# Performance work log

Hardware: AMD Instinct MI355X
Metric: run time of the kernel (lower is better)

## Reference

```python
import jax, jax.numpy as jnp
import numpy as np

B, N, DH = 8, 2048, 512
EPS = 1e-5


def _layer_norm(x, g, b):
    m = x.mean(-1, keepdims=True)
    v = ((x - m) ** 2).mean(-1, keepdims=True)
    return (x - m) * jax.lax.rsqrt(v + EPS) * g + b


def setup_inputs() -> dict:
    key = jax.random.key(0)
    ks = jax.random.split(key, 20)
    s = 1.0 / np.sqrt(DH)
    sf = 1.0 / np.sqrt(2 * DH)
    return {
        "H": jax.random.normal(ks[0], (B, N, DH), jnp.float32),
        "adj": jax.random.uniform(ks[1], (B, N, N), jnp.float32),
        "hop_emb": jax.random.normal(ks[2], (N, DH), jnp.float32),
        "Wq": jax.random.normal(ks[3], (DH, DH), jnp.float32) * s,
        "bq": jnp.zeros((DH,), jnp.float32),
        "Wk": jax.random.normal(ks[4], (DH, DH), jnp.float32) * s,
        "bk": jnp.zeros((DH,), jnp.float32),
        "Wv": jax.random.normal(ks[5], (DH, DH), jnp.float32) * s,
        "bv": jnp.zeros((DH,), jnp.float32),
        "W1": jax.random.normal(ks[6], (DH, 2 * DH), jnp.float32) * s,
        "b1": jnp.zeros((2 * DH,), jnp.float32),
        "W2": jax.random.normal(ks[7], (2 * DH, DH), jnp.float32) * sf,
        "b2": jnp.zeros((DH,), jnp.float32),
        "g1": jnp.ones((DH,), jnp.float32),
        "be1": jnp.zeros((DH,), jnp.float32),
        "g2": jnp.ones((DH,), jnp.float32),
        "be2": jnp.zeros((DH,), jnp.float32),
    }


def reference(H, adj, hop_emb, Wq, bq, Wk, bk, Wv, bv, W1, b1, W2, b2, g1, be1, g2, be2):
    Q = H @ Wq + bq                                     # [B,N,DH]
    K = H @ Wk + bk
    V = H @ Wv + bv
    scores = jnp.einsum("bid,bjd->bij", Q, K) / np.sqrt(DH).astype(np.float32)
    # (adj[...,None] * hop_emb).mean(-1) == adj * hop_emb.mean(-1)[j]
    hop_effect = adj * hop_emb.mean(-1)[None, None, :]  # [B,N,N]
    attn = jax.nn.softmax(scores * hop_effect, axis=-1)
    attn_out = jnp.einsum("bij,bjd->bid", attn, V)
    x = _layer_norm(attn_out + H, g1, be1)
    ffn = jax.nn.relu(x @ W1 + b1) @ W2 + b2
    return _layer_norm(ffn + x, g2, be2)
```

## Files before the change

### kernel.cpp

```cpp
#include <hip/hip_runtime.h>

typedef unsigned short u16;
typedef __bf16 bf16x8 __attribute__((ext_vector_type(8)));
typedef float f32x4 __attribute__((ext_vector_type(4)));

#define SEQN 2048
#define DHID 512

static __device__ __forceinline__ float bf2f(u16 u) {
    union { unsigned int i; float f; } c; c.i = ((unsigned int)u) << 16; return c.f;
}
static __device__ __forceinline__ u16 f2bf(float f) {
    union { float f; unsigned int i; } c; c.f = f;
    unsigned int x = c.i;
    return (u16)((x + 0x7fffu + ((x >> 16) & 1u)) >> 16);
}

static __device__ __forceinline__ void gld_lds16(const u16* g, u16* l) {
    __builtin_amdgcn_global_load_lds(
        (__attribute__((address_space(1))) void*)(g),
        (__attribute__((address_space(3))) void*)(l), 16, 0, 0);
}

__global__ __launch_bounds__(256) void cvt_kernel(const float* __restrict__ src,
                                                  u16* __restrict__ dst, int n) {
    int i = (blockIdx.x * 256 + threadIdx.x) * 8;
    if (i >= n) return;
    float4 a = *(const float4*)(src + i);
    float4 b = *(const float4*)(src + i + 4);
    union { uint4 u; u16 s[8]; } o;
    o.s[0] = f2bf(a.x); o.s[1] = f2bf(a.y); o.s[2] = f2bf(a.z); o.s[3] = f2bf(a.w);
    o.s[4] = f2bf(b.x); o.s[5] = f2bf(b.y); o.s[6] = f2bf(b.z); o.s[7] = f2bf(b.w);
    *(uint4*)(dst + i) = o.u;
}

__global__ __launch_bounds__(256) void cvt_t_kernel(const float* __restrict__ src,
                                                    u16* __restrict__ dst, int K, int N) {
    int idx = blockIdx.x * 256 + threadIdx.x;
    if (idx >= K * N) return;
    int n = idx / K, k = idx - n * K;
    dst[idx] = f2bf(src[(size_t)k * N + n]);
}

__global__ void hmean_kernel(const float* __restrict__ hop, float* __restrict__ hm) {
    int j = blockIdx.x, t = threadIdx.x;
    const float* p = hop + (size_t)j * DHID + t * 8;
    float4 a = *(const float4*)p;
    float4 b = *(const float4*)(p + 4);
    float s = a.x + a.y + a.z + a.w + b.x + b.y + b.z + b.w;
#pragma unroll
    for (int m = 1; m < 64; m <<= 1) s += __shfl_xor(s, m);
    if (t == 0) hm[j] = s * (1.0f / (float)DHID);
}

enum { EPI_BIAS = 0, EPI_RELU = 1, EPI_PLAIN = 3, EPI_BIAS_T = 4 };

template <int EPI>
__global__ __launch_bounds__(256) void gemm_bt(
    const u16* __restrict__ A, const u16* __restrict__ Bt, u16* __restrict__ C,
    const float* __restrict__ bias,
    int K, int lda, int ldb, int ldc,
    long sA, long sB, long sC)
{
    __shared__ u16 As[128 * 32];
    __shared__ u16 Bs[128 * 32];

    const int tid = threadIdx.x;
    const int bz = blockIdx.z;
    const u16* Ab = A + (size_t)bz * sA;
    const u16* Bb = Bt + (size_t)bz * sB;
    u16* Cb = C + (size_t)bz * sC;

    const int bm0 = blockIdx.y * 128, bn0 = blockIdx.x * 128;
    const int wid = tid >> 6, lane = tid & 63, quad = lane >> 4, l16 = lane & 15;
    const int wm = (wid >> 1) * 64, wn = (wid & 1) * 64;
    const int srow = lane >> 2;
    const int skof = (lane & 3) * 8;

    f32x4 acc[4][4];
#pragma unroll
    for (int i = 0; i < 4; ++i)
#pragma unroll
        for (int j = 0; j < 4; ++j) acc[i][j] = (f32x4){0.f, 0.f, 0.f, 0.f};

    for (int k0 = 0; k0 < K; k0 += 32) {
#pragma unroll
        for (int it = 0; it < 2; ++it) {
            int c = wid * 2 + it;
            gld_lds16(Ab + (size_t)(bm0 + c * 16 + srow) * lda + k0 + skof,
                      &As[c * 512]);
        }
#pragma unroll
        for (int it = 0; it < 2; ++it) {
            int c = wid * 2 + it;
            gld_lds16(Bb + (size_t)(bn0 + c * 16 + srow) * ldb + k0 + skof,
                      &Bs[c * 512]);
        }
        __syncthreads();

        bf16x8 af[4], bfr[4];
#pragma unroll
        for (int i = 0; i < 4; ++i)
            af[i] = *(const bf16x8*)&As[(wm + i * 16 + l16) * 32 + quad * 8];
#pragma unroll
        for (int j = 0; j < 4; ++j)
            bfr[j] = *(const bf16x8*)&Bs[(wn + j * 16 + l16) * 32 + quad * 8];
#pragma unroll
        for (int i = 0; i < 4; ++i)
#pragma unroll
            for (int j = 0; j < 4; ++j)
                acc[i][j] = __builtin_amdgcn_mfma_f32_16x16x32_bf16(af[i], bfr[j], acc[i][j], 0, 0, 0);
        __syncthreads();
    }

#pragma unroll
    for (int i = 0; i < 4; ++i) {
#pragma unroll
        for (int j = 0; j < 4; ++j) {
            const int gn = bn0 + wn + j * 16 + l16;
            const int gm0 = bm0 + wm + i * 16 + quad * 4;
            if constexpr (EPI == EPI_BIAS || EPI == EPI_RELU) {
                const float b = bias[gn];
#pragma unroll
                for (int r = 0; r < 4; ++r) {
                    float v = acc[i][j][r] + b;
                    if constexpr (EPI == EPI_RELU) v = fmaxf(v, 0.f);
                    Cb[(size_t)(gm0 + r) * ldc + gn] = f2bf(v);
                }
            } else if constexpr (EPI == EPI_BIAS_T) {
                const float b = bias[gn];
                const int bb = gm0 >> 11, n = gm0 & 2047;
                ushort4 o;
                o.x = f2bf(acc[i][j][0] + b);
                o.y = f2bf(acc[i][j][1] + b);
                o.z = f2bf(acc[i][j][2] + b);
                o.w = f2bf(acc[i][j][3] + b);
                *(ushort4*)&C[((size_t)bb * 512 + gn) * 2048 + n] = o;
            } else {
#pragma unroll
                for (int r = 0; r < 4; ++r)
                    Cb[(size_t)(gm0 + r) * ldc + gn] = f2bf(acc[i][j][r]);
            }
        }
    }
}

__global__ __launch_bounds__(256, 1) void attn_kernel(
    const u16* __restrict__ Q, const u16* __restrict__ K, const u16* __restrict__ Vt,
    const float* __restrict__ adj, const float* __restrict__ hm,
    u16* __restrict__ AO)
{
    extern __shared__ u16 lds[];
    u16* Ks = lds;
    u16* Vs = lds + 16384;

    const int tid = threadIdx.x, wid = tid >> 6, lane = tid & 63;
    const int quad = lane >> 4, l16 = lane & 15;
    const int b = blockIdx.x;
    const int q0w = blockIdx.y * 64 + wid * 16;
    const int srow = lane >> 2, sko = (lane & 3) * 8;

    const u16* Qg = Q + (size_t)b * SEQN * DHID;
    const u16* Kg = K + (size_t)b * SEQN * DHID;
    const u16* Vg = Vt + (size_t)b * DHID * SEQN;
    const float* adjg = adj + (size_t)b * SEQN * SEQN;
    u16* AOg = AO + (size_t)b * SEQN * DHID;
    u16* Plds = lds + wid * 640;

    const float scale = 0.044194173824159216f;

    bf16x8 qf[16];
#pragma unroll
    for (int ds = 0; ds < 16; ++ds)
        qf[ds] = *(const bf16x8*)(Qg + (size_t)(q0w + l16) * DHID + ds * 32 + quad * 8);

    f32x4 oacc[32];
#pragma unroll
    for (int dt = 0; dt < 32; ++dt) oacc[dt] = (f32x4){0.f, 0.f, 0.f, 0.f};
    float lsum[4] = {0.f, 0.f, 0.f, 0.f};

    for (int kt = 0; kt < 64; ++kt) {
        const int kv0 = kt * 32;

#pragma unroll
        for (int i = 0; i < 8; ++i) {
            int id = wid * 8 + i;
            int ds = id >> 1, c = id & 1;
            gld_lds16(Kg + (size_t)(kv0 + c * 16 + srow) * DHID + ds * 32 + sko,
                      &Ks[ds * 1024 + c * 512]);
        }
        __syncthreads();

#pragma unroll
        for (int i = 0; i < 8; ++i) {
            int id = wid * 8 + i;
            gld_lds16(Vg + (size_t)(id * 16 + srow) * SEQN + kv0 + sko,
                      &Vs[id * 512]);
        }

        float hv0 = hm[kv0 + l16] * scale;
        float hv1 = hm[kv0 + 16 + l16] * scale;
        float av[8];
        const float* arow = adjg + (size_t)(q0w + quad * 4) * SEQN + kv0;
#pragma unroll
        for (int r = 0; r < 4; ++r) {
            av[r]     = arow[(size_t)r * SEQN + l16];
            av[4 + r] = arow[(size_t)r * SEQN + 16 + l16];
        }

        f32x4 s0a = {0.f,0.f,0.f,0.f}, s0b = {0.f,0.f,0.f,0.f};
        f32x4 s1a = {0.f,0.f,0.f,0.f}, s1b = {0.f,0.f,0.f,0.f};
#pragma unroll
        for (int ds = 0; ds < 16; ds += 2) {
            bf16x8 k00 = *(const bf16x8*)&Ks[ds * 1024 + l16 * 32 + quad * 8];
            bf16x8 k01 = *(const bf16x8*)&Ks[ds * 1024 + 512 + l16 * 32 + quad * 8];
            s0a = __builtin_amdgcn_mfma_f32_16x16x32_bf16(qf[ds], k00, s0a, 0, 0, 0);
            s1a = __builtin_amdgcn_mfma_f32_16x16x32_bf16(qf[ds], k01, s1a, 0, 0, 0);
            bf16x8 k10 = *(const bf16x8*)&Ks[(ds + 1) * 1024 + l16 * 32 + quad * 8];
            bf16x8 k11 = *(const bf16x8*)&Ks[(ds + 1) * 1024 + 512 + l16 * 32 + quad * 8];
            s0b = __builtin_amdgcn_mfma_f32_16x16x32_bf16(qf[ds + 1], k10, s0b, 0, 0, 0);
            s1b = __builtin_amdgcn_mfma_f32_16x16x32_bf16(qf[ds + 1], k11, s1b, 0, 0, 0);
        }
        f32x4 s0 = s0a + s0b, s1 = s1a + s1b;
        __syncthreads();

#pragma unroll
        for (int r = 0; r < 4; ++r) {
            float p0 = __expf(s0[r] * av[r] * hv0);
            float p1 = __expf(s1[r] * av[4 + r] * hv1);
            lsum[r] += p0 + p1;
            Plds[(quad * 4 + r) * 40 + l16] = f2bf(p0);
            Plds[(quad * 4 + r) * 40 + 16 + l16] = f2bf(p1);
        }
        asm volatile("s_waitcnt lgkmcnt(0)" ::: "memory");

        bf16x8 pf = *(const bf16x8*)&Plds[l16 * 40 + quad * 8];
#pragma unroll
        for (int dt = 0; dt < 32; ++dt) {
            bf16x8 vf = *(const bf16x8*)&Vs[(dt * 16 + l16) * 32 + quad * 8];
            oacc[dt] = __builtin_amdgcn_mfma_f32_16x16x32_bf16(pf, vf, oacc[dt], 0, 0, 0);
        }
        __syncthreads();
    }

#pragma unroll
    for (int r = 0; r < 4; ++r) {
#pragma unroll
        for (int m = 1; m < 16; m <<= 1) lsum[r] += __shfl_xor(lsum[r], m);
        lsum[r] = 1.f / lsum[r];
    }
#pragma unroll
    for (int dt = 0; dt < 32; ++dt) {
#pragma unroll
        for (int r = 0; r < 4; ++r) {
            AOg[(size_t)(q0w + quad * 4 + r) * DHID + dt * 16 + l16] =
                f2bf(oacc[dt][r] * lsum[r]);
        }
    }
}

template <bool B_F32, bool OUT_F32>
__global__ __launch_bounds__(256) void ln_kernel(
    const u16* __restrict__ a, const void* __restrict__ bp,
    const float* __restrict__ g, const float* __restrict__ be,
    void* __restrict__ out)
{
    size_t row = blockIdx.x;
    int t = threadIdx.x, wid = t >> 6, lane = t & 63;
    const u16* pa = a + row * (size_t)DHID;

    unsigned int va = *(const unsigned int*)(pa + t * 2);
    float b0, b1;
    if constexpr (B_F32) {
        float2 vb = *(const float2*)((const float*)bp + row * (size_t)DHID + t * 2);
        b0 = vb.x; b1 = vb.y;
    } else {
        unsigned int vb = *(const unsigned int*)((const u16*)bp + row * (size_t)DHID + t * 2);
        b0 = bf2f((u16)(vb & 0xffff)); b1 = bf2f((u16)(vb >> 16));
    }
    float x0 = bf2f((u16)(va & 0xffff)) + b0;
    float x1 = bf2f((u16)(va >> 16)) + b1;
    float s = x0 + x1, sq = x0 * x0 + x1 * x1;
#pragma unroll
    for (int m = 1; m < 64; m <<= 1) { s += __shfl_xor(s, m); sq += __shfl_xor(sq, m); }
    __shared__ float rs[4], rq[4];
    if (lane == 0) { rs[wid] = s; rq[wid] = sq; }
    __syncthreads();
    s = rs[0] + rs[1] + rs[2] + rs[3];
    sq = rq[0] + rq[1] + rq[2] + rq[3];
    float mean = s * (1.f / (float)DHID);
    float var = sq * (1.f / (float)DHID) - mean * mean;
    float rstd = rsqrtf(var + 1e-5f);

    float2 vg = *(const float2*)(g + t * 2);
    float2 vbe = *(const float2*)(be + t * 2);
    float y0 = (x0 - mean) * rstd * vg.x + vbe.x;
    float y1 = (x1 - mean) * rstd * vg.y + vbe.y;
    if constexpr (OUT_F32) {
        *(float2*)((float*)out + row * (size_t)DHID + t * 2) = make_float2(y0, y1);
    } else {
        unsigned int o = (unsigned int)f2bf(y0) | ((unsigned int)f2bf(y1) << 16);
        *(unsigned int*)((u16*)out + row * (size_t)DHID + t * 2) = o;
    }
}

extern "C" void kernel_launch(void* const* d_in, const int* in_sizes, int n_in,
                              void* d_out, int out_size, void* d_ws, size_t ws_size,
                              hipStream_t stream) {
    const float* H   = (const float*)d_in[0];
    const float* adj = (const float*)d_in[1];
    const float* hop = (const float*)d_in[2];
    const float* Wq  = (const float*)d_in[3];
    const float* bq  = (const float*)d_in[4];
    const float* Wk  = (const float*)d_in[5];
    const float* bk  = (const float*)d_in[6];
    const float* Wv  = (const float*)d_in[7];
    const float* bv  = (const float*)d_in[8];
    const float* W1  = (const float*)d_in[9];
    const float* b1  = (const float*)d_in[10];
    const float* W2  = (const float*)d_in[11];
    const float* b2  = (const float*)d_in[12];
    const float* g1  = (const float*)d_in[13];
    const float* be1 = (const float*)d_in[14];
    const float* g2  = (const float*)d_in[15];
    const float* be2 = (const float*)d_in[16];

    const size_t MiB = 1ull << 20;
    char* w = (char*)d_ws;
    float* hm  = (float*)w;
    u16* Hb   = (u16*)(w + 1 * MiB);
    u16* Wqt  = (u16*)(w + 17 * MiB);
    u16* Wkt  = (u16*)(w + 17 * MiB + 512 * 1024);
    u16* Wvt  = (u16*)(w + 18 * MiB);
    u16* W1t  = (u16*)(w + 18 * MiB + 512 * 1024);
    u16* W2t  = (u16*)(w + 19 * MiB + 512 * 1024);
    u16* Q    = (u16*)(w + 21 * MiB);
    u16* Kb   = (u16*)(w + 37 * MiB);
    u16* Vt   = (u16*)(w + 53 * MiB);
    u16* AO   = (u16*)(w + 69 * MiB);
    u16* HID  = (u16*)(w + 85 * MiB);
    u16* X   = Kb;
    u16* F2  = Vt;

    const int BN = 8, N = SEQN, D = DHID;
    const long nd = (long)N * D;

    cvt_kernel<<<(BN * N * D) / (8 * 256), 256, 0, stream>>>(H, Hb, BN * N * D);
    cvt_t_kernel<<<(D * D + 255) / 256, 256, 0, stream>>>(Wq, Wqt, D, D);
    cvt_t_kernel<<<(D * D + 255) / 256, 256, 0, stream>>>(Wk, Wkt, D, D);
    cvt_t_kernel<<<(D * D + 255) / 256, 256, 0, stream>>>(Wv, Wvt, D, D);
    cvt_t_kernel<<<(D * 2 * D + 255) / 256, 256, 0, stream>>>(W1, W1t, D, 2 * D);
    cvt_t_kernel<<<(2 * D * D + 255) / 256, 256, 0, stream>>>(W2, W2t, 2 * D, D);

    hmean_kernel<<<N, 64, 0, stream>>>(hop, hm);

    gemm_bt<EPI_BIAS><<<dim3(4, 128, 1), 256, 0, stream>>>(
        Hb, Wqt, Q, bq, D, D, D, D, 0, 0, 0);
    gemm_bt<EPI_BIAS><<<dim3(4, 128, 1), 256, 0, stream>>>(
        Hb, Wkt, Kb, bk, D, D, D, D, 0, 0, 0);
    gemm_bt<EPI_BIAS_T><<<dim3(4, 128, 1), 256, 0, stream>>>(
        Hb, Wvt, Vt, bv, D, D, D, D, 0, 0, 0);

    attn_kernel<<<dim3(8, 32), 256, 65536, stream>>>(Q, Kb, Vt, adj, hm, AO);

    ln_kernel<true, false><<<BN * N, 256, 0, stream>>>(AO, H, g1, be1, X);

    gemm_bt<EPI_RELU><<<dim3(8, 128, 1), 256, 0, stream>>>(
        X, W1t, HID, b1, D, D, D, 2 * D, 0, 0, 0);

    gemm_bt<EPI_BIAS><<<dim3(4, 128, 1), 256, 0, stream>>>(
        HID, W2t, F2, b2, 2 * D, 2 * D, 2 * D, D, 0, 0, 0);

    ln_kernel<false, true><<<BN * N, 256, 0, stream>>>(F2, X, g2, be2, (float*)d_out);
}
```

Measured before the change: 595.9 us.

## Fuse QKV projections into one GEMM and split attention over two KV halves

The three Q/K/V projection GEMMs become a single GEMM over a concatenated transposed weight, with an epilogue that routes each column tile to Q, K or transposed V. The attention kernel gets a second grid dimension that splits the key/value range in half. Each half writes unnormalized partial outputs and row sums, and the first LayerNorm kernel adds the halves and normalizes them. This is meant to double the number of attention blocks for better CU utilization and to cut launch and A-reload overhead for the projections. In exchange it adds extra partial-output traffic to global memory, and more blocks may not help if register or LDS use limits occupancy to one block per CU.

Measured after the change: 595.5 us. Within noise of the previous version (-0.1%).

```diff
diff --git a/kernel.cpp b/kernel.cpp
--- a/kernel.cpp
+++ b/kernel.cpp
@@ -53,23 +53,23 @@
     if (t == 0) hm[j] = s * (1.0f / (float)DHID);
 }
 
-enum { EPI_BIAS = 0, EPI_RELU = 1, EPI_PLAIN = 3, EPI_BIAS_T = 4 };
+enum { EPI_BIAS = 0, EPI_RELU = 1, EPI_PLAIN = 3, EPI_BIAS_T = 4, EPI_QKV = 5 };
 
 template <int EPI>
 __global__ __launch_bounds__(256) void gemm_bt(
     const u16* __restrict__ A, const u16* __restrict__ Bt, u16* __restrict__ C,
     const float* __restrict__ bias,
     int K, int lda, int ldb, int ldc,
-    long sA, long sB, long sC)
+    u16* __restrict__ Qo, u16* __restrict__ Ko, u16* __restrict__ Vto,
+    const float* __restrict__ bq_, const float* __restrict__ bk_,
+    const float* __restrict__ bv_)
 {
     __shared__ u16 As[128 * 32];
     __shared__ u16 Bs[128 * 32];
 
     const int tid = threadIdx.x;
-    const int bz = blockIdx.z;
-    const u16* Ab = A + (size_t)bz * sA;
-    const u16* Bb = Bt + (size_t)bz * sB;
-    u16* Cb = C + (size_t)bz * sC;
+    const u16* Ab = A;
+    const u16* Bb = Bt;
 
     const int bm0 = blockIdx.y * 128, bn0 = blockIdx.x * 128;
     const int wid = tid >> 6, lane = tid & 63, quad = lane >> 4, l16 = lane & 15;
@@ -125,7 +125,7 @@
                 for (int r = 0; r < 4; ++r) {
                     float v = acc[i][j][r] + b;
                     if constexpr (EPI == EPI_RELU) v = fmaxf(v, 0.f);
-                    Cb[(size_t)(gm0 + r) * ldc + gn] = f2bf(v);
+                    C[(size_t)(gm0 + r) * ldc + gn] = f2bf(v);
                 }
             } else if constexpr (EPI == EPI_BIAS_T) {
                 const float b = bias[gn];
@@ -136,10 +136,33 @@
                 o.z = f2bf(acc[i][j][2] + b);
                 o.w = f2bf(acc[i][j][3] + b);
                 *(ushort4*)&C[((size_t)bb * 512 + gn) * 2048 + n] = o;
+            } else if constexpr (EPI == EPI_QKV) {
+                const int sel = gn >> 9;
+                const int n = gn & 511;
+                if (sel == 0) {
+                    const float b = bq_[n];
+#pragma unroll
+                    for (int r = 0; r < 4; ++r)
+                        Qo[(size_t)(gm0 + r) * DHID + n] = f2bf(acc[i][j][r] + b);
+                } else if (sel == 1) {
+                    const float b = bk_[n];
+#pragma unroll
+                    for (int r = 0; r < 4; ++r)
+                        Ko[(size_t)(gm0 + r) * DHID + n] = f2bf(acc[i][j][r] + b);
+                } else {
+                    const float b = bv_[n];
+                    const int bb = gm0 >> 11, nn2 = gm0 & 2047;
+                    ushort4 o;
+                    o.x = f2bf(acc[i][j][0] + b);
+                    o.y = f2bf(acc[i][j][1] + b);
+                    o.z = f2bf(acc[i][j][2] + b);
+                    o.w = f2bf(acc[i][j][3] + b);
+                    *(ushort4*)&Vto[((size_t)bb * 512 + n) * 2048 + nn2] = o;
+                }
             } else {
 #pragma unroll
                 for (int r = 0; r < 4; ++r)
-                    Cb[(size_t)(gm0 + r) * ldc + gn] = f2bf(acc[i][j][r]);
+                    C[(size_t)(gm0 + r) * ldc + gn] = f2bf(acc[i][j][r]);
             }
         }
     }
@@ -148,7 +171,7 @@
 __global__ __launch_bounds__(256, 1) void attn_kernel(
     const u16* __restrict__ Q, const u16* __restrict__ K, const u16* __restrict__ Vt,
     const float* __restrict__ adj, const float* __restrict__ hm,
-    u16* __restrict__ AO)
+    u16* __restrict__ Opart, float* __restrict__ Lpart)
 {
     extern __shared__ u16 lds[];
     u16* Ks = lds;
@@ -158,13 +181,14 @@
     const int quad = lane >> 4, l16 = lane & 15;
     const int b = blockIdx.x;
     const int q0w = blockIdx.y * 64 + wid * 16;
+    const int z = blockIdx.z;
     const int srow = lane >> 2, sko = (lane & 3) * 8;
 
     const u16* Qg = Q + (size_t)b * SEQN * DHID;
     const u16* Kg = K + (size_t)b * SEQN * DHID;
     const u16* Vg = Vt + (size_t)b * DHID * SEQN;
     const float* adjg = adj + (size_t)b * SEQN * SEQN;
-    u16* AOg = AO + (size_t)b * SEQN * DHID;
+    u16* Og = Opart + ((size_t)z * 8 + b) * SEQN * DHID;
     u16* Plds = lds + wid * 640;
 
     const float scale = 0.044194173824159216f;
@@ -179,8 +203,8 @@
     for (int dt = 0; dt < 32; ++dt) oacc[dt] = (f32x4){0.f, 0.f, 0.f, 0.f};
     float lsum[4] = {0.f, 0.f, 0.f, 0.f};
 
-    for (int kt = 0; kt < 64; ++kt) {
-        const int kv0 = kt * 32;
+    for (int kt = 0; kt < 32; ++kt) {
+        const int kv0 = z * 1024 + kt * 32;
 
 #pragma unroll
         for (int i = 0; i < 8; ++i) {
@@ -247,39 +271,36 @@
     for (int r = 0; r < 4; ++r) {
 #pragma unroll
         for (int m = 1; m < 16; m <<= 1) lsum[r] += __shfl_xor(lsum[r], m);
-        lsum[r] = 1.f / lsum[r];
+        if (l16 == 0)
+            Lpart[(size_t)z * 16384 + b * 2048 + q0w + quad * 4 + r] = lsum[r];
     }
 #pragma unroll
     for (int dt = 0; dt < 32; ++dt) {
 #pragma unroll
         for (int r = 0; r < 4; ++r) {
-            AOg[(size_t)(q0w + quad * 4 + r) * DHID + dt * 16 + l16] =
-                f2bf(oacc[dt][r] * lsum[r]);
+            Og[(size_t)(q0w + quad * 4 + r) * DHID + dt * 16 + l16] =
+                f2bf(oacc[dt][r]);
         }
     }
 }
 
-template <bool B_F32, bool OUT_F32>
-__global__ __launch_bounds__(256) void ln_kernel(
-    const u16* __restrict__ a, const void* __restrict__ bp,
+__global__ __launch_bounds__(256) void ln_comb_kernel(
+    const u16* __restrict__ O1, const u16* __restrict__ O2,
+    const float* __restrict__ L1, const float* __restrict__ L2,
+    const float* __restrict__ Hf,
     const float* __restrict__ g, const float* __restrict__ be,
-    void* __restrict__ out)
+    u16* __restrict__ out)
 {
     size_t row = blockIdx.x;
     int t = threadIdx.x, wid = t >> 6, lane = t & 63;
-    const u16* pa = a + row * (size_t)DHID;
-
-    unsigned int va = *(const unsigned int*)(pa + t * 2);
-    float b0, b1;
-    if constexpr (B_F32) {
-        float2 vb = *(const float2*)((const float*)bp + row * (size_t)DHID + t * 2);
-        b0 = vb.x; b1 = vb.y;
-    } else {
-        unsigned int vb = *(const unsigned int*)((const u16*)bp + row * (size_t)DHID + t * 2);
-        b0 = bf2f((u16)(vb & 0xffff)); b1 = bf2f((u16)(vb >> 16));
-    }
-    float x0 = bf2f((u16)(va & 0xffff)) + b0;
-    float x1 = bf2f((u16)(va >> 16)) + b1;
+    float sc = 1.f / (L1[row] + L2[row]);
+
+    unsigned int a1 = *(const unsigned int*)(O1 + row * (size_t)DHID + t * 2);
+    unsigned int a2 = *(const unsigned int*)(O2 + row * (size_t)DHID + t * 2);
+    float2 h = *(const float2*)(Hf + row * (size_t)DHID + t * 2);
+    float x0 = (bf2f((u16)(a1 & 0xffff)) + bf2f((u16)(a2 & 0xffff))) * sc + h.x;
+    float x1 = (bf2f((u16)(a1 >> 16)) + bf2f((u16)(a2 >> 16))) * sc + h.y;
+
     float s = x0 + x1, sq = x0 * x0 + x1 * x1;
 #pragma unroll
     for (int m = 1; m < 64; m <<= 1) { s += __shfl_xor(s, m); sq += __shfl_xor(sq, m); }
@@ -296,12 +317,37 @@
     float2 vbe = *(const float2*)(be + t * 2);
     float y0 = (x0 - mean) * rstd * vg.x + vbe.x;
     float y1 = (x1 - mean) * rstd * vg.y + vbe.y;
-    if constexpr (OUT_F32) {
-        *(float2*)((float*)out + row * (size_t)DHID + t * 2) = make_float2(y0, y1);
-    } else {
-        unsigned int o = (unsigned int)f2bf(y0) | ((unsigned int)f2bf(y1) << 16);
-        *(unsigned int*)((u16*)out + row * (size_t)DHID + t * 2) = o;
-    }
+    unsigned int o = (unsigned int)f2bf(y0) | ((unsigned int)f2bf(y1) << 16);
+    *(unsigned int*)(out + row * (size_t)DHID + t * 2) = o;
+}
+
+__global__ __launch_bounds__(256) void ln_kernel_f32out(
+    const u16* __restrict__ a, const u16* __restrict__ bp,
+    const float* __restrict__ g, const float* __restrict__ be,
+    float* __restrict__ out)
+{
+    size_t row = blockIdx.x;
+    int t = threadIdx.x, wid = t >> 6, lane = t & 63;
+    unsigned int va = *(const unsigned int*)(a + row * (size_t)DHID + t * 2);
+    unsigned int vb = *(const unsigned int*)(bp + row * (size_t)DHID + t * 2);
+    float x0 = bf2f((u16)(va & 0xffff)) + bf2f((u16)(vb & 0xffff));
+    float x1 = bf2f((u16)(va >> 16)) + bf2f((u16)(vb >> 16));
+    float s = x0 + x1, sq = x0 * x0 + x1 * x1;
+#pragma unroll
+    for (int m = 1; m < 64; m <<= 1) { s += __shfl_xor(s, m); sq += __shfl_xor(sq, m); }
+    __shared__ float rs[4], rq[4];
+    if (lane == 0) { rs[wid] = s; rq[wid] = sq; }
+    __syncthreads();
+    s = rs[0] + rs[1] + rs[2] + rs[3];
+    sq = rq[0] + rq[1] + rq[2] + rq[3];
+    float mean = s * (1.f / (float)DHID);
+    float var = sq * (1.f / (float)DHID) - mean * mean;
+    float rstd = rsqrtf(var + 1e-5f);
+    float2 vg = *(const float2*)(g + t * 2);
+    float2 vbe = *(const float2*)(be + t * 2);
+    float y0 = (x0 - mean) * rstd * vg.x + vbe.x;
+    float y1 = (x1 - mean) * rstd * vg.y + vbe.y;
+    *(float2*)(out + row * (size_t)DHID + t * 2) = make_float2(y0, y1);
 }
 
 extern "C" void kernel_launch(void* const* d_in, const int* in_sizes, int n_in,
@@ -327,49 +373,46 @@
 
     const size_t MiB = 1ull << 20;
     char* w = (char*)d_ws;
-    float* hm  = (float*)w;
-    u16* Hb   = (u16*)(w + 1 * MiB);
-    u16* Wqt  = (u16*)(w + 17 * MiB);
-    u16* Wkt  = (u16*)(w + 17 * MiB + 512 * 1024);
-    u16* Wvt  = (u16*)(w + 18 * MiB);
-    u16* W1t  = (u16*)(w + 18 * MiB + 512 * 1024);
-    u16* W2t  = (u16*)(w + 19 * MiB + 512 * 1024);
-    u16* Q    = (u16*)(w + 21 * MiB);
-    u16* Kb   = (u16*)(w + 37 * MiB);
-    u16* Vt   = (u16*)(w + 53 * MiB);
-    u16* AO   = (u16*)(w + 69 * MiB);
-    u16* HID  = (u16*)(w + 85 * MiB);
+    float* hm   = (float*)w;
+    float* Lp   = (float*)(w + 256 * 1024);
+    u16* Hb    = (u16*)(w + 1 * MiB);
+    u16* Wqkvt = (u16*)(w + 17 * MiB);
+    u16* W1t   = (u16*)(w + 18 * MiB + 512 * 1024);
+    u16* W2t   = (u16*)(w + 19 * MiB + 512 * 1024);
+    u16* Q     = (u16*)(w + 21 * MiB);
+    u16* Kb    = (u16*)(w + 37 * MiB);
+    u16* Vt    = (u16*)(w + 53 * MiB);
+    u16* O1    = (u16*)(w + 69 * MiB);
+    u16* O2    = (u16*)(w + 85 * MiB);
+    u16* HID   = (u16*)(w + 101 * MiB);
     u16* X   = Kb;
     u16* F2  = Vt;
 
     const int BN = 8, N = SEQN, D = DHID;
-    const long nd = (long)N * D;
 
     cvt_kernel<<<(BN * N * D) / (8 * 256), 256, 0, stream>>>(H, Hb, BN * N * D);
-    cvt_t_kernel<<<(D * D + 255) / 256, 256, 0, stream>>>(Wq, Wqt, D, D);
-    cvt_t_kernel<<<(D * D + 255) / 256, 256, 0, stream>>>(Wk, Wkt, D, D);
-    cvt_t_kernel<<<(D * D + 255) / 256, 256, 0, stream>>>(Wv, Wvt, D, D);
+    cvt_t_kernel<<<(D * D + 255) / 256, 256, 0, stream>>>(Wq, Wqkvt, D, D);
+    cvt_t_kernel<<<(D * D + 255) / 256, 256, 0, stream>>>(Wk, Wqkvt + D * D, D, D);
+    cvt_t_kernel<<<(D * D + 255) / 256, 256, 0, stream>>>(Wv, Wqkvt + 2 * D * D, D, D);
     cvt_t_kernel<<<(D * 2 * D + 255) / 256, 256, 0, stream>>>(W1, W1t, D, 2 * D);
     cvt_t_kernel<<<(2 * D * D + 255) / 256, 256, 0, stream>>>(W2, W2t, 2 * D, D);
 
     hmean_kernel<<<N, 64, 0, stream>>>(hop, hm);
 
+    gemm_bt<EPI_QKV><<<dim3(12, 128, 1), 256, 0, stream>>>(
+        Hb, Wqkvt, nullptr, nullptr, D, D, D, 0, Q, Kb, Vt, bq, bk, bv);
+
+    attn_kernel<<<dim3(8, 32, 2), 256, 65536, stream>>>(
+        Q, Kb, Vt, adj, hm, O1, Lp);
+
+    ln_comb_kernel<<<BN * N, 256, 0, stream>>>(
+        O1, O2, Lp, Lp + 16384, H, g1, be1, X);
+
+    gemm_bt<EPI_RELU><<<dim3(8, 128, 1), 256, 0, stream>>>(
+        X, W1t, HID, b1, D, D, D, 2 * D, nullptr, nullptr, nullptr, nullptr, nullptr, nullptr);
+
     gemm_bt<EPI_BIAS><<<dim3(4, 128, 1), 256, 0, stream>>>(
-        Hb, Wqt, Q, bq, D, D, D, D, 0, 0, 0);
-    gemm_bt<EPI_BIAS><<<dim3(4, 128, 1), 256, 0, stream>>>(
-        Hb, Wkt, Kb, bk, D, D, D, D, 0, 0, 0);
-    gemm_bt<EPI_BIAS_T><<<dim3(4, 128, 1), 256, 0, stream>>>(
-        Hb, Wvt, Vt, bv, D, D, D, D, 0, 0, 0);
-
-    attn_kernel<<<dim3(8, 32), 256, 65536, stream>>>(Q, Kb, Vt, adj, hm, AO);
-
-    ln_kernel<true, false><<<BN * N, 256, 0, stream>>>(AO, H, g1, be1, X);
-
-    gemm_bt<EPI_RELU><<<dim3(8, 128, 1), 256, 0, stream>>>(
-        X, W1t, HID, b1, D, D, D, 2 * D, 0, 0, 0);
-
-    gemm_bt<EPI_BIAS><<<dim3(4, 128, 1), 256, 0, stream>>>(
-        HID, W2t, F2, b2, 2 * D, 2 * D, 2 * D, D, 0, 0, 0);
-
-    ln_kernel<false, true><<<BN * N, 256, 0, stream>>>(F2, X, g2, be2, (float*)d_out);
-}
+        HID, W2t, F2, b2, 2 * D, 2 * D, 2 * D, D, nullptr, nullptr, nullptr, nullptr, nullptr, nullptr);
+
+    ln_kernel_f32out<<<BN * N, 256, 0, stream>>>(F2, X, g2, be2, (float*)d_out);
+}
```
